# Performance work log

Hardware: AMD Instinct MI355X
Metric: run time of the kernel (lower is better)

The kernel has to match this reference:

```python
import jax, jax.numpy as jnp
import numpy as np

E, D, H, T = 8, 1024, 4096, 8192


def setup_inputs() -> dict:
    key = jax.random.key(0)
    k1, k2, k3 = jax.random.split(key, 3)
    inp = jax.random.normal(k1, (T, D), dtype=jnp.float32)
    w1 = jax.random.normal(k2, (E, H, D), dtype=jnp.float32) * (D ** -0.5)
    b1 = jnp.zeros((E, H), dtype=jnp.float32)
    w2 = jax.random.normal(k3, (E, D, H), dtype=jnp.float32) * (H ** -0.5)
    b2 = jnp.zeros((E, D), dtype=jnp.float32)
    fwd_expert_count = jnp.full((E,), T // E, dtype=jnp.int32)
    return {"inp": inp, "w1": w1, "b1": b1, "w2": w2, "b2": b2,
            "fwd_expert_count": fwd_expert_count}


def _grouped_linear(x, w, b, eid):
    # x: [T, in], w: [E, out, in], b: [E, out], eid: [T] expert id per token.
    # Tokens are contiguous per expert; we compute each expert's GEMM and
    # mask-select the rows belonging to that expert (small fixed E loop).
    out = jnp.zeros((x.shape[0], w.shape[1]), dtype=x.dtype)
    for e in range(w.shape[0]):
        mask = (eid == e)[:, None]
        out = out + jnp.where(mask, x @ w[e].T + b[e], jnp.zeros((), x.dtype))
    return out


def reference(inp, w1, b1, w2, b2, fwd_expert_count):
    # Map each (sorted) token to its expert via cumulative segment bounds.
    bounds = jnp.cumsum(fwd_expert_count)            # [E]
    eid = jnp.searchsorted(bounds, jnp.arange(inp.shape[0]), side="right")  # [T]
    h = _grouped_linear(inp, w1, b1, eid)            # [T, H]  itoh
    h = jax.nn.gelu(h, approximate=False)            # activation
    out = _grouped_linear(h, w2, b2, eid)            # [T, D]  htoi
    return out
```

## Files before the change

kernel.cpp:

```cpp
#include <hip/hip_runtime.h>
#include <hip/hip_bf16.h>
#include <cstdint>
#include <cstddef>


typedef __bf16 bf16x8 __attribute__((ext_vector_type(8)));
typedef float f32x4 __attribute__((ext_vector_type(4)));
typedef unsigned short u16x8 __attribute__((ext_vector_type(8)));

#define BM 128
#define BN 128

__device__ __forceinline__ unsigned short f2bf(float f) {
  unsigned u = __builtin_bit_cast(unsigned, f);
  u += 0x7FFFu + ((u >> 16) & 1u);
  return (unsigned short)(u >> 16);
}

__device__ __forceinline__ float fast_gelu(float v) {
  const float u = 0.7978845608028654f * (v + 0.044715f * v * v * v);
  const float t = 1.0f - 2.0f / (__expf(2.0f * u) + 1.0f);
  return 0.5f * v * (1.0f + t);
}

__device__ __forceinline__ void gload16(const void* g, void* lds) {
  __builtin_amdgcn_global_load_lds(
      (const __attribute__((address_space(1))) void*)g,
      (__attribute__((address_space(3))) void*)lds, 16, 0, 0);
}

__device__ __forceinline__ void cvt8(const float* __restrict__ src,
                                     unsigned short* __restrict__ dst, long i) {
  float4 a = *reinterpret_cast<const float4*>(src + i);
  float4 b = *reinterpret_cast<const float4*>(src + i + 4);
  u16x8 o;
  o[0] = f2bf(a.x); o[1] = f2bf(a.y); o[2] = f2bf(a.z); o[3] = f2bf(a.w);
  o[4] = f2bf(b.x); o[5] = f2bf(b.y); o[6] = f2bf(b.z); o[7] = f2bf(b.w);
  *reinterpret_cast<u16x8*>(dst + i) = o;
}

__global__ void cvt2_build(const float* __restrict__ s0,
                           unsigned short* __restrict__ d0, long n0,
                           const float* __restrict__ s1,
                           unsigned short* __restrict__ d1, long n1,
                           const int* __restrict__ cnt, int E,
                           int4* __restrict__ tbl, int* __restrict__ ntp) {
  if (blockIdx.x == 0 && threadIdx.x == 0) {
    int nt = 0, start = 0;
    for (int e = 0; e < E; ++e) {
      int c = cnt[e];
      for (int t = 0; t < c; t += BM) {
        int4 v; v.x = e; v.y = start + t; v.z = (c - t < BM ? c - t : BM); v.w = 0;
        tbl[nt++] = v;
      }
      start += c;
    }
    *ntp = nt;
  }
  long i = ((long)blockIdx.x * blockDim.x + threadIdx.x) * 8;
  const long stride = (long)gridDim.x * blockDim.x * 8;
  const long ntot = n0 + n1;
  for (; i < ntot; i += stride) {
    if (i < n0) cvt8(s0, d0, i);
    else        cvt8(s1, d1, i - n0);
  }
}

template <int GELU, int OUTBF, int PIGGY, int BKT>
__global__ __launch_bounds__(256, 2) void grouped_gemm(
    const unsigned short* __restrict__ A, const unsigned short* __restrict__ W,
    const float* __restrict__ bias, void* __restrict__ Cv,
    const int4* __restrict__ tbl, const int* __restrict__ ntp,
    const int N, const int K,
    const float* __restrict__ pg_src, unsigned short* __restrict__ pg_dst,
    const long pg_n, const int yTiles) {
  if (PIGGY && (int)blockIdx.y >= yTiles) {
    const int p = ((int)blockIdx.y - yTiles) * gridDim.x + blockIdx.x;
    const long PB = (long)(gridDim.y - yTiles) * gridDim.x;
    long i = ((long)p * blockDim.x + threadIdx.x) * 8;
    const long stride = PB * blockDim.x * 8;
    for (; i < pg_n; i += stride) cvt8(pg_src, pg_dst, i);
    return;
  }

  const int mt = blockIdx.y;
  const int bx = blockIdx.x;
  if (mt >= *ntp) return;
  const int4 ti = tbl[mt];
  const int e = ti.x, row0 = ti.y, rows = ti.z;
  const int bcol = bx * BN;

  __shared__ alignas(16) unsigned short sA[2][BM * BKT];
  __shared__ alignas(16) unsigned short sB[2][BN * BKT];

  const int tid = threadIdx.x;
  const int lane = tid & 63;
  const int wave = tid >> 6;
  const int wr = wave >> 1;
  const int wc = wave & 1;
  const int lr = lane & 15;
  const int lhi = lane >> 4;

  const unsigned short* __restrict__ Wexp = W + (size_t)e * N * K;

  constexpr int CH  = BKT / 8;
  constexpr int LPM = BKT / 16;
  constexpr int RPL = 2048 / BKT;
  const int srow = wave * (512 / BKT) + (BKT == 32 ? (lane >> 2) : (lane >> 3));
  const int chn = lane & (CH - 1);
  int cg;
  if constexpr (BKT == 32) cg = chn ^ ((srow >> 1) & 3);
  else                     cg = chn ^ (srow & 7);

  const unsigned short* gA[LPM];
  const unsigned short* gB[LPM];
#pragma unroll
  for (int i = 0; i < LPM; ++i) {
    const int rA = srow + i * RPL;
    const int rc = rA < rows ? rA : rows - 1;
    gA[i] = A + (size_t)(row0 + rc) * K + cg * 8;
    gB[i] = Wexp + (size_t)(bcol + srow + i * RPL) * K + cg * 8;
  }

  auto stage = [&](int kt, int b) {
    char* da = (char*)&sA[b][0] + wave * 1024;
    char* db = (char*)&sB[b][0] + wave * 1024;
#pragma unroll
    for (int i = 0; i < LPM; ++i) {
      gload16(gA[i] + kt * BKT, da + i * 4096);
      gload16(gB[i] + kt * BKT, db + i * 4096);
    }
  };

  constexpr int KH = BKT / 32;
  int swo[KH];
  if constexpr (BKT == 32) {
    swo[0] = (lhi ^ ((lr >> 1) & 3)) * 8;
  } else {
    swo[0] = (lhi ^ (lr & 7)) * 8;
    swo[1] = ((4 | lhi) ^ (lr & 7)) * 8;
  }
  const int aRowB = wr * 64 + lr;
  const int bRowB = wc * 64 + lr;

  f32x4 acc[4][4] = {};
  const int nk = K / BKT;

  stage(0, 0);
  __syncthreads();

  int buf = 0;
  for (int t = 0; t < nk; ++t) {
    if (t + 1 < nk) stage(t + 1, buf ^ 1);
    bf16x8 af[4][KH], bfr[4][KH];
#pragma unroll
    for (int m = 0; m < 4; ++m) {
      const unsigned short* rp = &sA[buf][(aRowB + m * 16) * BKT];
#pragma unroll
      for (int kh = 0; kh < KH; ++kh)
        af[m][kh] = *reinterpret_cast<const bf16x8*>(rp + swo[kh]);
    }
#pragma unroll
    for (int n = 0; n < 4; ++n) {
      const unsigned short* rp = &sB[buf][(bRowB + n * 16) * BKT];
#pragma unroll
      for (int kh = 0; kh < KH; ++kh)
        bfr[n][kh] = *reinterpret_cast<const bf16x8*>(rp + swo[kh]);
    }
#pragma unroll
    for (int kh = 0; kh < KH; ++kh)
#pragma unroll
      for (int m = 0; m < 4; ++m)
#pragma unroll
        for (int n = 0; n < 4; ++n)
          acc[m][n] = __builtin_amdgcn_mfma_f32_16x16x32_bf16(
              af[m][kh], bfr[n][kh], acc[m][n], 0, 0, 0);
    __syncthreads();
    buf ^= 1;
  }

  const float* __restrict__ be = bias + (size_t)e * N;
  const int colBase = bcol + wc * 64 + lr;
  const int rowBase = wr * 64 + (lhi << 2);
#pragma unroll
  for (int n = 0; n < 4; ++n) {
    const int col = colBase + n * 16;
    const float bv = be[col];
#pragma unroll
    for (int m = 0; m < 4; ++m) {
      const int r0 = rowBase + m * 16;
#pragma unroll
      for (int j = 0; j < 4; ++j) {
        const int rr = r0 + j;
        if (rr < rows) {
          float v = acc[m][n][j] + bv;
          if (GELU) v = fast_gelu(v);
          const size_t idx = (size_t)(row0 + rr) * N + col;
          if (OUTBF) ((unsigned short*)Cv)[idx] = f2bf(v);
          else       ((float*)Cv)[idx] = v;
        }
      }
    }
  }
}

extern "C" void kernel_launch(void* const* d_in, const int* in_sizes, int n_in,
                              void* d_out, int out_size, void* d_ws, size_t ws_size,
                              hipStream_t stream) {
  const float* inp = (const float*)d_in[0];
  const float* w1  = (const float*)d_in[1];
  const float* b1  = (const float*)d_in[2];
  const float* w2  = (const float*)d_in[3];
  const float* b2  = (const float*)d_in[4];
  const int*   cnt = (const int*)d_in[5];

  const int E = in_sizes[5];
  const int H = in_sizes[2] / E;
  const int D = in_sizes[4] / E;
  const int T = in_sizes[0] / D;

  char* ws = (char*)d_ws;
  int4* tbl = (int4*)ws;
  int* ntp = (int*)(ws + 2048);
  size_t off = 4096;
  unsigned short* inp_bf = (unsigned short*)(ws + off); off += (size_t)T * D * 2;
  unsigned short* w1_bf  = (unsigned short*)(ws + off); off += (size_t)E * H * D * 2;
  unsigned short* w2_bf  = (unsigned short*)(ws + off); off += (size_t)E * D * H * 2;
  unsigned short* h_bf   = (unsigned short*)(ws + off); off += (size_t)T * H * 2;
  (void)ws_size; (void)n_in; (void)out_size;

  cvt2_build<<<2048, 256, 0, stream>>>(inp, inp_bf, (long)T * D,
                                       w1, w1_bf, (long)E * H * D,
                                       cnt, E, tbl, ntp);

  const int maxTiles = T / BM + E;
  dim3 g1(H / BN, maxTiles + 8);
  grouped_gemm<1, 1, 1, 32><<<g1, 256, 0, stream>>>(
      inp_bf, w1_bf, b1, h_bf, tbl, ntp, H, D,
      w2, w2_bf, (long)E * D * H, maxTiles);
  dim3 g2(D / BN, maxTiles);
  grouped_gemm<0, 0, 0, 64><<<g2, 256, 0, stream>>>(
      h_bf, w2_bf, b2, d_out, tbl, ntp, D, H,
      nullptr, nullptr, 0, maxTiles);
}
```

Measured before the change: 306.2 us.

## Use single A buffer with BK=64 in first GEMM to raise occupancy

The first grouped GEMM moves from a 32-wide K tile to a 64-wide one. It keeps A in a single shared-memory buffer while B stays double-buffered, which frees LDS so launch bounds can target three blocks per CU. Because the A buffer is shared, the prefetch of the next tile now happens after a barrier, once the fragments are in registers. This trades less overlap of global loads with MFMA for higher occupancy and fewer K iterations. The second GEMM's inner loop now loads LDS fragments per K-half, which lowers register pressure.

New measurement: 308.2 us. About the same (+0.7%).

```diff
diff --git a/kernel.cpp b/kernel.cpp
--- a/kernel.cpp
+++ b/kernel.cpp
@@ -66,14 +66,15 @@
   }
 }
 
-template <int GELU, int OUTBF, int PIGGY, int BKT>
-__global__ __launch_bounds__(256, 2) void grouped_gemm(
+template <int GELU, int OUTBF, int PIGGY, int SINGLEA, int WPE>
+__global__ __launch_bounds__(256, WPE) void grouped_gemm(
     const unsigned short* __restrict__ A, const unsigned short* __restrict__ W,
     const float* __restrict__ bias, void* __restrict__ Cv,
     const int4* __restrict__ tbl, const int* __restrict__ ntp,
     const int N, const int K,
     const float* __restrict__ pg_src, unsigned short* __restrict__ pg_dst,
     const long pg_n, const int yTiles) {
+  constexpr int BKT = 64;
   if (PIGGY && (int)blockIdx.y >= yTiles) {
     const int p = ((int)blockIdx.y - yTiles) * gridDim.x + blockIdx.x;
     const long PB = (long)(gridDim.y - yTiles) * gridDim.x;
@@ -90,7 +91,7 @@
   const int e = ti.x, row0 = ti.y, rows = ti.z;
   const int bcol = bx * BN;
 
-  __shared__ alignas(16) unsigned short sA[2][BM * BKT];
+  __shared__ alignas(16) unsigned short sA[SINGLEA ? 1 : 2][BM * BKT];
   __shared__ alignas(16) unsigned short sB[2][BN * BKT];
 
   const int tid = threadIdx.x;
@@ -106,11 +107,9 @@
   constexpr int CH  = BKT / 8;
   constexpr int LPM = BKT / 16;
   constexpr int RPL = 2048 / BKT;
-  const int srow = wave * (512 / BKT) + (BKT == 32 ? (lane >> 2) : (lane >> 3));
+  const int srow = wave * 8 + (lane >> 3);
   const int chn = lane & (CH - 1);
-  int cg;
-  if constexpr (BKT == 32) cg = chn ^ ((srow >> 1) & 3);
-  else                     cg = chn ^ (srow & 7);
+  const int cg = chn ^ (srow & (CH - 1));
 
   const unsigned short* gA[LPM];
   const unsigned short* gB[LPM];
@@ -122,9 +121,9 @@
     gB[i] = Wexp + (size_t)(bcol + srow + i * RPL) * K + cg * 8;
   }
 
-  auto stage = [&](int kt, int b) {
-    char* da = (char*)&sA[b][0] + wave * 1024;
-    char* db = (char*)&sB[b][0] + wave * 1024;
+  auto stage = [&](int kt, int bA, int bB) {
+    char* da = (char*)&sA[bA][0] + wave * 1024;
+    char* db = (char*)&sB[bB][0] + wave * 1024;
 #pragma unroll
     for (int i = 0; i < LPM; ++i) {
       gload16(gA[i] + kt * BKT, da + i * 4096);
@@ -134,49 +133,73 @@
 
   constexpr int KH = BKT / 32;
   int swo[KH];
-  if constexpr (BKT == 32) {
-    swo[0] = (lhi ^ ((lr >> 1) & 3)) * 8;
-  } else {
-    swo[0] = (lhi ^ (lr & 7)) * 8;
-    swo[1] = ((4 | lhi) ^ (lr & 7)) * 8;
-  }
+#pragma unroll
+  for (int kh = 0; kh < KH; ++kh)
+    swo[kh] = ((kh * 4 + lhi) ^ (lr & (CH - 1))) * 8;
   const int aRowB = wr * 64 + lr;
   const int bRowB = wc * 64 + lr;
 
   f32x4 acc[4][4] = {};
   const int nk = K / BKT;
 
-  stage(0, 0);
+  stage(0, 0, 0);
   __syncthreads();
 
   int buf = 0;
-  for (int t = 0; t < nk; ++t) {
-    if (t + 1 < nk) stage(t + 1, buf ^ 1);
-    bf16x8 af[4][KH], bfr[4][KH];
-#pragma unroll
-    for (int m = 0; m < 4; ++m) {
-      const unsigned short* rp = &sA[buf][(aRowB + m * 16) * BKT];
+  if constexpr (SINGLEA) {
+    for (int t = 0; t < nk; ++t) {
+      bf16x8 af[4][KH], bfr[4][KH];
+#pragma unroll
+      for (int m = 0; m < 4; ++m) {
+        const unsigned short* rp = &sA[0][(aRowB + m * 16) * BKT];
+#pragma unroll
+        for (int kh = 0; kh < KH; ++kh)
+          af[m][kh] = *reinterpret_cast<const bf16x8*>(rp + swo[kh]);
+      }
+#pragma unroll
+      for (int n = 0; n < 4; ++n) {
+        const unsigned short* rp = &sB[buf][(bRowB + n * 16) * BKT];
+#pragma unroll
+        for (int kh = 0; kh < KH; ++kh)
+          bfr[n][kh] = *reinterpret_cast<const bf16x8*>(rp + swo[kh]);
+      }
+      __syncthreads();
+      if (t + 1 < nk) stage(t + 1, 0, buf ^ 1);
 #pragma unroll
       for (int kh = 0; kh < KH; ++kh)
-        af[m][kh] = *reinterpret_cast<const bf16x8*>(rp + swo[kh]);
-    }
-#pragma unroll
-    for (int n = 0; n < 4; ++n) {
-      const unsigned short* rp = &sB[buf][(bRowB + n * 16) * BKT];
-#pragma unroll
-      for (int kh = 0; kh < KH; ++kh)
-        bfr[n][kh] = *reinterpret_cast<const bf16x8*>(rp + swo[kh]);
-    }
-#pragma unroll
-    for (int kh = 0; kh < KH; ++kh)
-#pragma unroll
-      for (int m = 0; m < 4; ++m)
+#pragma unroll
+        for (int m = 0; m < 4; ++m)
+#pragma unroll
+          for (int n = 0; n < 4; ++n)
+            acc[m][n] = __builtin_amdgcn_mfma_f32_16x16x32_bf16(
+                af[m][kh], bfr[n][kh], acc[m][n], 0, 0, 0);
+      __syncthreads();
+      buf ^= 1;
+    }
+  } else {
+    for (int t = 0; t < nk; ++t) {
+      if (t + 1 < nk) stage(t + 1, buf ^ 1, buf ^ 1);
+#pragma unroll
+      for (int kh = 0; kh < KH; ++kh) {
+        bf16x8 af[4], bfr[4];
+#pragma unroll
+        for (int m = 0; m < 4; ++m)
+          af[m] = *reinterpret_cast<const bf16x8*>(
+              &sA[buf][(aRowB + m * 16) * BKT + swo[kh]]);
 #pragma unroll
         for (int n = 0; n < 4; ++n)
-          acc[m][n] = __builtin_amdgcn_mfma_f32_16x16x32_bf16(
-              af[m][kh], bfr[n][kh], acc[m][n], 0, 0, 0);
-    __syncthreads();
-    buf ^= 1;
+          bfr[n] = *reinterpret_cast<const bf16x8*>(
+              &sB[buf][(bRowB + n * 16) * BKT + swo[kh]]);
+#pragma unroll
+        for (int m = 0; m < 4; ++m)
+#pragma unroll
+          for (int n = 0; n < 4; ++n)
+            acc[m][n] = __builtin_amdgcn_mfma_f32_16x16x32_bf16(
+                af[m], bfr[n], acc[m][n], 0, 0, 0);
+      }
+      __syncthreads();
+      buf ^= 1;
+    }
   }
 
   const float* __restrict__ be = bias + (size_t)e * N;
@@ -235,11 +258,11 @@
 
   const int maxTiles = T / BM + E;
   dim3 g1(H / BN, maxTiles + 8);
-  grouped_gemm<1, 1, 1, 32><<<g1, 256, 0, stream>>>(
+  grouped_gemm<1, 1, 1, 1, 3><<<g1, 256, 0, stream>>>(
       inp_bf, w1_bf, b1, h_bf, tbl, ntp, H, D,
       w2, w2_bf, (long)E * D * H, maxTiles);
   dim3 g2(D / BN, maxTiles);
-  grouped_gemm<0, 0, 0, 64><<<g2, 256, 0, stream>>>(
+  grouped_gemm<0, 0, 0, 0, 2><<<g2, 256, 0, stream>>>(
       h_bf, w2_bf, b2, d_out, tbl, ntp, D, H,
       nullptr, nullptr, 0, maxTiles);
 }
```
